# Optimization experiments

Hardware: AMD Instinct MI355X
Metric: run time of the kernel (lower is better)

The kernel has to match this reference:

```python
import jax, jax.numpy as jnp
import numpy as np

DIM = 768
N_HEADS = 12
HEAD_DIM = DIM // N_HEADS
HIDDEN = int(DIM * 4.0)
B, S = 4, 2048
EPS = 1e-6
SCALE = HEAD_DIM ** -0.5


def layer_norm(x, gamma, beta):
    mu = jnp.mean(x, axis=-1, keepdims=True)
    var = jnp.mean((x - mu) ** 2, axis=-1, keepdims=True)
    return (x - mu) * jax.lax.rsqrt(var + EPS) * gamma + beta


def setup_inputs() -> dict:
    key = jax.random.key(0)
    ks = jax.random.split(key, 8)
    x = jax.random.normal(ks[0], (B, S, DIM), dtype=jnp.float32)
    mask = jax.random.randint(ks[1], (B, 1, S, S), 0, 2, dtype=jnp.int32)
    sd = DIM ** -0.5
    return {
        "x": x,
        "mask": mask,
        "w_qkv": jax.random.normal(ks[2], (DIM, 3 * DIM), dtype=jnp.float32) * sd,
        "b_qkv": jnp.zeros((3 * DIM,), jnp.float32),
        "w_proj": jax.random.normal(ks[3], (DIM, DIM), dtype=jnp.float32) * sd,
        "b_proj": jnp.zeros((DIM,), jnp.float32),
        "g1": jnp.ones((DIM,), jnp.float32),
        "beta1": jnp.zeros((DIM,), jnp.float32),
        "g2": jnp.ones((DIM,), jnp.float32),
        "beta2": jnp.zeros((DIM,), jnp.float32),
        "w1": jax.random.normal(ks[4], (DIM, HIDDEN), dtype=jnp.float32) * sd,
        "b1": jnp.zeros((HIDDEN,), jnp.float32),
        "w2": jax.random.normal(ks[5], (HIDDEN, DIM), dtype=jnp.float32) * (HIDDEN ** -0.5),
        "b2": jnp.zeros((DIM,), jnp.float32),
    }


def reference(x, mask, w_qkv, b_qkv, w_proj, b_proj, g1, beta1, g2, beta2, w1, b1, w2, b2):
    # --- attention branch (pre-LN) ---
    h = layer_norm(x, g1, beta1)
    qkv = h @ w_qkv + b_qkv                              # (B,S,3*DIM)
    qkv = qkv.reshape(B, S, 3, N_HEADS, HEAD_DIM)
    q, k, v = (qkv[:, :, 0], qkv[:, :, 1], qkv[:, :, 2])  # (B,S,H,D)
    # scores: (B,H,S,S) -- materialized like the original
    dp = jnp.einsum("bqhd,bkhd->bhqk", q, k) * SCALE
    dp = jnp.where(mask == 0, jnp.float32(-10000.0), dp)
    attn = jax.nn.softmax(dp, axis=-1)
    wa = jnp.einsum("bhqk,bkhd->bqhd", attn, v).reshape(B, S, DIM)
    x = x + (wa @ w_proj + b_proj)
    # --- MLP branch (pre-LN) ---
    h = layer_norm(x, g2, beta2)
    h = jax.nn.gelu(h @ w1 + b1, approximate=False)
    x = x + (h @ w2 + b2)
    return x
```

## Files before the change

### kernel.cpp

```cpp
#include <hip/hip_runtime.h>
#include <hip/hip_bf16.h>
#include <math.h>

typedef __bf16 bf16;
typedef __bf16 bf16x8 __attribute__((ext_vector_type(8)));
typedef short bf16x4s __attribute__((ext_vector_type(4)));
typedef float f32x4 __attribute__((ext_vector_type(4)));

#define DIM 768
#define NH 12
#define HD 64
#define HID 3072
#define BB 4
#define SS 2048
#define QPRESCALE 0.18033688011112042f

#define MFMA(a, b, c) __builtin_amdgcn_mfma_f32_16x16x32_bf16(a, b, c, 0, 0, 0)
#define MFMA16(a, b, c) \
  __builtin_amdgcn_mfma_f32_16x16x16bf16_1k(a, b, c, 0, 0, 0)

__device__ __forceinline__ void gld16(const void* g, void* l) {
  __builtin_amdgcn_global_load_lds(
      (const __attribute__((address_space(1))) void*)g,
      (__attribute__((address_space(3))) void*)l, 16, 0, 0);
}

__device__ __forceinline__ unsigned pk2(float a, float b) {
  union {
    bf16 h[2];
    unsigned u;
  } t;
  t.h[0] = (bf16)a;
  t.h[1] = (bf16)b;
  return t.u;
}

__global__ __launch_bounds__(256) void castT_all_kernel(
    const float* __restrict__ s0, bf16* __restrict__ d0,
    const float* __restrict__ s1, bf16* __restrict__ d1,
    const float* __restrict__ s2, bf16* __restrict__ d2,
    const float* __restrict__ s3, bf16* __restrict__ d3) {
  __shared__ float tile[32][33];
  int id = blockIdx.x;
  const float* in;
  bf16* out;
  int R, C, loc;
  if (id < 1728) { in = s0; out = d0; R = 768; C = 2304; loc = id; }
  else if (id < 2304) { in = s1; out = d1; R = 768; C = 768; loc = id - 1728; }
  else if (id < 4608) { in = s2; out = d2; R = 768; C = 3072; loc = id - 2304; }
  else { in = s3; out = d3; R = 3072; C = 768; loc = id - 4608; }
  const int cb = C >> 5;
  const int c0 = (loc % cb) * 32, r0 = (loc / cb) * 32;
  const int tx = threadIdx.x & 31, ty = threadIdx.x >> 5;
#pragma unroll
  for (int i = 0; i < 32; i += 8)
    tile[ty + i][tx] = in[(size_t)(r0 + ty + i) * C + c0 + tx];
  __syncthreads();
#pragma unroll
  for (int i = 0; i < 32; i += 8)
    out[(size_t)(c0 + ty + i) * R + r0 + tx] = (bf16)tile[tx][ty + i];
}

__global__ __launch_bounds__(256) void maskbits_kernel(
    const int* __restrict__ mask, unsigned* __restrict__ bits) {
  const int i = blockIdx.x * 256 + threadIdx.x;
  unsigned long long m = __ballot(mask[i] != 0);
  const int lane = threadIdx.x & 63;
  if (lane == 0) bits[i >> 5] = (unsigned)m;
  else if (lane == 32) bits[i >> 5] = (unsigned)(m >> 32);
}

__global__ __launch_bounds__(256) void ln_kernel(
    const float* __restrict__ x, const float* __restrict__ g,
    const float* __restrict__ beta, bf16* __restrict__ out) {
  const int row = blockIdx.x, t = threadIdx.x;
  const float* xr = x + (size_t)row * DIM;
  float v0 = xr[t], v1 = xr[t + 256], v2 = xr[t + 512];
  float s = v0 + v1 + v2;
  float s2 = v0 * v0 + v1 * v1 + v2 * v2;
#pragma unroll
  for (int d = 1; d < 64; d <<= 1) {
    s += __shfl_xor(s, d);
    s2 += __shfl_xor(s2, d);
  }
  __shared__ float red[8];
  const int wv = t >> 6, lane = t & 63;
  if (lane == 0) { red[wv] = s; red[wv + 4] = s2; }
  __syncthreads();
  s = red[0] + red[1] + red[2] + red[3];
  s2 = red[4] + red[5] + red[6] + red[7];
  const float mu = s * (1.0f / DIM);
  const float var = s2 * (1.0f / DIM) - mu * mu;
  const float r = rsqrtf(var + 1e-6f);
  bf16* o = out + (size_t)row * DIM;
  o[t] = (bf16)((v0 - mu) * r * g[t] + beta[t]);
  o[t + 256] = (bf16)((v1 - mu) * r * g[t + 256] + beta[t + 256]);
  o[t + 512] = (bf16)((v2 - mu) * r * g[t + 512] + beta[t + 512]);
}

enum { EPI_QKV = 0, EPI_PROJ = 1, EPI_FFN1 = 2, EPI_FFN2 = 3 };

template <int EPI, int K>
__global__ __launch_bounds__(256) void gemm_kernel(
    const bf16* __restrict__ A, const bf16* __restrict__ Bt,
    const float* __restrict__ bias, const float* __restrict__ res,
    void* __restrict__ o0, void* __restrict__ o1, void* __restrict__ o2) {
  constexpr int NIT = K / 64;
  __shared__ bf16 As[2][128 * 64];
  __shared__ bf16 Bs[2][64 * 64];
  const int tid = threadIdx.x;
  const int wv = tid >> 6, lane = tid & 63;
  const int quad = lane >> 4, l15 = lane & 15;
  const int lrow = lane >> 3, lcol = lane & 7;
  const int m0 = blockIdx.y * 128, n0 = blockIdx.x * 64;
  const int wm = wv * 32;

  f32x4 acc[2][4] = {};

  const int swz = (lcol ^ lrow) * 8;
  const bf16* Ag = A + (size_t)(m0 + wv * 32 + lrow) * K + swz;
  const bf16* Bg = Bt + (size_t)(n0 + wv * 16 + lrow) * K + swz;

  auto stage = [&](int buf, int k0) {
#pragma unroll
    for (int i = 0; i < 4; i++)
      gld16(Ag + (size_t)(i * 8) * K + k0, &As[buf][(wv * 32 + i * 8) * 64]);
#pragma unroll
    for (int i = 0; i < 2; i++)
      gld16(Bg + (size_t)(i * 8) * K + k0,
            &Bs[buf][(wv * 16 + i * 8) * 64]);
  };

  stage(0, 0);

  for (int it = 0; it < NIT; ++it) {
    __syncthreads();
    if (it + 1 < NIT) stage((it + 1) & 1, (it + 1) * 64);
    const bf16* Ab = As[it & 1];
    const bf16* Bb = Bs[it & 1];
#pragma unroll
    for (int ks = 0; ks < 2; ks++) {
      bf16x8 af[2], bfr[4];
#pragma unroll
      for (int i = 0; i < 2; i++) {
        const int ra = wm + i * 16 + l15;
        af[i] = *(const bf16x8*)&Ab[ra * 64 + ((ks * 4 + quad) ^ (ra & 7)) * 8];
      }
#pragma unroll
      for (int i = 0; i < 4; i++) {
        const int rb = i * 16 + l15;
        bfr[i] =
            *(const bf16x8*)&Bb[rb * 64 + ((ks * 4 + quad) ^ (rb & 7)) * 8];
      }
#pragma unroll
      for (int mi = 0; mi < 2; mi++)
#pragma unroll
        for (int ni = 0; ni < 4; ni++)
          acc[mi][ni] = MFMA(af[mi], bfr[ni], acc[mi][ni]);
    }
  }

#pragma unroll
  for (int mi = 0; mi < 2; mi++) {
#pragma unroll
    for (int ni = 0; ni < 4; ni++) {
      const int n = n0 + ni * 16 + l15;
      const float bv = bias[n];
      const int mb = m0 + wm + mi * 16 + quad * 4;
      float val[4];
#pragma unroll
      for (int r = 0; r < 4; r++) val[r] = acc[mi][ni][r] + bv;
      if (EPI == EPI_QKV) {
        const int which = n / 768;
        const int nn = n - which * 768;
        const int hh = nn >> 6, d = nn & 63;
        const int bb = mb >> 11, s = mb & 2047;
        if (which == 0) {
#pragma unroll
          for (int r = 0; r < 4; r++)
            ((bf16*)o0)[((size_t)(bb * NH + hh) * SS + s + r) * HD + d] =
                (bf16)(val[r] * QPRESCALE);
        } else if (which == 1) {
#pragma unroll
          for (int r = 0; r < 4; r++)
            ((bf16*)o1)[((size_t)(bb * NH + hh) * SS + s + r) * HD + d] =
                (bf16)val[r];
        } else {
          uint2 pv;
          pv.x = pk2(val[0], val[1]);
          pv.y = pk2(val[2], val[3]);
          *(uint2*)&((bf16*)o2)[((size_t)(bb * NH + hh) * HD + d) * SS + s] = pv;
        }
      } else if (EPI == EPI_PROJ) {
#pragma unroll
        for (int r = 0; r < 4; r++)
          ((float*)o0)[(size_t)(mb + r) * DIM + n] =
              res[(size_t)(mb + r) * DIM + n] + val[r];
      } else if (EPI == EPI_FFN1) {
#pragma unroll
        for (int r = 0; r < 4; r++) {
          const float ge =
              0.5f * val[r] * (1.0f + erff(val[r] * 0.70710678118654752f));
          ((bf16*)o0)[(size_t)(mb + r) * HID + n] = (bf16)ge;
        }
      } else {
#pragma unroll
        for (int r = 0; r < 4; r++)
          ((float*)o0)[(size_t)(mb + r) * DIM + n] =
              res[(size_t)(mb + r) * DIM + n] + val[r];
      }
    }
  }
}

__global__ __launch_bounds__(256) void attn_kernel(
    const bf16* __restrict__ q, const bf16* __restrict__ k,
    const bf16* __restrict__ vT, const unsigned* __restrict__ bits,
    bf16* __restrict__ wa) {
  const int b = blockIdx.z, h = blockIdx.y, q0 = blockIdx.x * 128;
  const int tid = threadIdx.x, wv = tid >> 6, lane = tid & 63;
  const int quad = lane >> 4, l15 = lane & 15;
  const int lrow = lane >> 3, lcol = lane & 7;

  __shared__ bf16 Ks[64 * 64];
  __shared__ bf16 Vs[64 * 64];
  __shared__ unsigned lut[32];

  if (tid < 16) {
    lut[2 * tid] =
        ((tid & 1) ? 0xFFFFu : 0u) | ((tid & 2) ? 0xFFFF0000u : 0u);
    lut[2 * tid + 1] =
        ((tid & 4) ? 0xFFFFu : 0u) | ((tid & 8) ? 0xFFFF0000u : 0u);
  }

  const bf16* qbh = q + (size_t)(b * NH + h) * SS * HD;
  const bf16* kbh = k + (size_t)(b * NH + h) * SS * HD;
  const bf16* vbh = vT + (size_t)(b * NH + h) * HD * SS;

  bf16x8 aq[2][2];
#pragma unroll
  for (int mi = 0; mi < 2; mi++)
#pragma unroll
    for (int ks = 0; ks < 2; ks++) {
      const int s = q0 + wv * 32 + mi * 16 + l15;
      aq[mi][ks] = *(const bf16x8*)&qbh[(size_t)s * HD + ks * 32 + quad * 8];
    }

  const unsigned long long* mrow[2];
#pragma unroll
  for (int mi = 0; mi < 2; mi++)
    mrow[mi] = (const unsigned long long*)bits +
               (size_t)(b * SS + q0 + wv * 32 + mi * 16 + l15) * 32;

  f32x4 O[2][4] = {};
  f32x4 lm[2] = {};
  const short oneb = 0x3F80;
  const bf16x4s onesA = {oneb, oneb, oneb, oneb};
  const int swz = (lcol ^ lrow) * 8;

  for (int t = 0; t < SS / 64; ++t) {
    const int s0 = t * 64;
#pragma unroll
    for (int i = 0; i < 2; i++) {
      const int r = wv * 16 + i * 8 + lrow;
      gld16(&kbh[(size_t)(s0 + r) * HD + swz], &Ks[(wv * 16 + i * 8) * 64]);
      gld16(&vbh[(size_t)r * SS + s0 + swz], &Vs[(wv * 16 + i * 8) * 64]);
    }
    const unsigned long long sh0 = mrow[0][t] >> (quad * 4);
    const unsigned long long sh1 = mrow[1][t] >> (quad * 4);
    const unsigned lo0 = (unsigned)sh0, hi0 = (unsigned)(sh0 >> 32);
    const unsigned lo1 = (unsigned)sh1, hi1 = (unsigned)(sh1 >> 32);
    __syncthreads();

#pragma unroll
    for (int ni = 0; ni < 4; ni++) {
      const int rr = ni * 16 + l15;
      const bf16x8 kf0 = *(const bf16x8*)&Ks[rr * 64 + (quad ^ (rr & 7)) * 8];
      const bf16x8 kf1 =
          *(const bf16x8*)&Ks[rr * 64 + ((4 + quad) ^ (rr & 7)) * 8];
      f32x4 a0 = {}, a1 = {};
      a0 = MFMA(kf0, aq[0][0], a0);
      a0 = MFMA(kf1, aq[0][1], a0);
      a1 = MFMA(kf0, aq[1][0], a1);
      a1 = MFMA(kf1, aq[1][1], a1);
      const unsigned nib0 = (ni == 0)   ? (lo0 & 0xF)
                            : (ni == 1) ? ((lo0 >> 16) & 0xF)
                            : (ni == 2) ? (hi0 & 0xF)
                                        : ((hi0 >> 16) & 0xF);
      const unsigned nib1 = (ni == 0)   ? (lo1 & 0xF)
                            : (ni == 1) ? ((lo1 >> 16) & 0xF)
                            : (ni == 2) ? (hi1 & 0xF)
                                        : ((hi1 >> 16) & 0xF);
      const uint2 mw0 = *(const uint2*)&lut[2 * nib0];
      const uint2 mw1 = *(const uint2*)&lut[2 * nib1];
      union {
        unsigned u[2];
        bf16x4s v;
      } p0, p1;
      p0.u[0] = pk2(__builtin_amdgcn_exp2f(a0[0]),
                    __builtin_amdgcn_exp2f(a0[1])) & mw0.x;
      p0.u[1] = pk2(__builtin_amdgcn_exp2f(a0[2]),
                    __builtin_amdgcn_exp2f(a0[3])) & mw0.y;
      p1.u[0] = pk2(__builtin_amdgcn_exp2f(a1[0]),
                    __builtin_amdgcn_exp2f(a1[1])) & mw1.x;
      p1.u[1] = pk2(__builtin_amdgcn_exp2f(a1[2]),
                    __builtin_amdgcn_exp2f(a1[3])) & mw1.y;
      lm[0] = MFMA16(onesA, p0.v, lm[0]);
      lm[1] = MFMA16(onesA, p1.v, lm[1]);
#pragma unroll
      for (int nd = 0; nd < 4; nd++) {
        const int row = nd * 16 + l15;
        const int pc = (ni * 2 + (quad >> 1)) ^ (row & 7);
        const bf16x4s vf =
            *(const bf16x4s*)&Vs[row * 64 + pc * 8 + (quad & 1) * 4];
        O[0][nd] = MFMA16(vf, p0.v, O[0][nd]);
        O[1][nd] = MFMA16(vf, p1.v, O[1][nd]);
      }
    }
    __syncthreads();
  }

#pragma unroll
  for (int mi = 0; mi < 2; mi++) {
    const float rln = __builtin_amdgcn_rcpf(lm[mi][0]);
    const int sq = q0 + wv * 32 + mi * 16 + l15;
    bf16* dst = wa + (size_t)(b * SS + sq) * DIM + h * HD + quad * 4;
#pragma unroll
    for (int nd = 0; nd < 4; nd++) {
      uint2 pv;
      pv.x = pk2(O[mi][nd][0] * rln, O[mi][nd][1] * rln);
      pv.y = pk2(O[mi][nd][2] * rln, O[mi][nd][3] * rln);
      *(uint2*)&dst[nd * 16] = pv;
    }
  }
}

extern "C" void kernel_launch(void* const* d_in, const int* in_sizes, int n_in,
                              void* d_out, int out_size, void* d_ws,
                              size_t ws_size, hipStream_t stream) {
  const float* x = (const float*)d_in[0];
  const int* mask = (const int*)d_in[1];
  const float* w_qkv = (const float*)d_in[2];
  const float* b_qkv = (const float*)d_in[3];
  const float* w_proj = (const float*)d_in[4];
  const float* b_proj = (const float*)d_in[5];
  const float* g1 = (const float*)d_in[6];
  const float* beta1 = (const float*)d_in[7];
  const float* g2 = (const float*)d_in[8];
  const float* beta2 = (const float*)d_in[9];
  const float* w1 = (const float*)d_in[10];
  const float* b1 = (const float*)d_in[11];
  const float* w2 = (const float*)d_in[12];
  const float* b2 = (const float*)d_in[13];
  float* out = (float*)d_out;

  char* p = (char*)d_ws;
  auto alloc = [&](size_t bytes) {
    char* r = p;
    p += (bytes + 1023) & ~(size_t)1023;
    return r;
  };
  bf16* wqkvT = (bf16*)alloc((size_t)2304 * 768 * 2);
  bf16* wprojT = (bf16*)alloc((size_t)768 * 768 * 2);
  bf16* w1T = (bf16*)alloc((size_t)3072 * 768 * 2);
  bf16* w2T = (bf16*)alloc((size_t)768 * 3072 * 2);
  unsigned* bits = (unsigned*)alloc((size_t)BB * SS * 64 * 4);
  bf16* h = (bf16*)alloc((size_t)8192 * 768 * 2);
  bf16* qb = (bf16*)alloc((size_t)8192 * 768 * 2);
  bf16* kb = (bf16*)alloc((size_t)8192 * 768 * 2);
  bf16* vtb = (bf16*)alloc((size_t)8192 * 768 * 2);
  bf16* wab = (bf16*)alloc((size_t)8192 * 768 * 2);
  float* x2 = (float*)alloc((size_t)8192 * 768 * 4);
  bf16* ffn1 = (bf16*)alloc((size_t)8192 * 3072 * 2);

  castT_all_kernel<<<6912, 256, 0, stream>>>(w_qkv, wqkvT, w_proj, wprojT, w1,
                                             w1T, w2, w2T);
  maskbits_kernel<<<(BB * SS * SS) / 256, 256, 0, stream>>>(mask, bits);
  ln_kernel<<<8192, 256, 0, stream>>>(x, g1, beta1, h);
  gemm_kernel<EPI_QKV, 768>
      <<<dim3(2304 / 64, 8192 / 128), 256, 0, stream>>>(h, wqkvT, b_qkv,
                                                        nullptr, qb, kb, vtb);
  attn_kernel<<<dim3(SS / 128, NH, BB), 256, 0, stream>>>(qb, kb, vtb, bits,
                                                          wab);
  gemm_kernel<EPI_PROJ, 768>
      <<<dim3(768 / 64, 8192 / 128), 256, 0, stream>>>(wab, wprojT, b_proj, x,
                                                       x2, nullptr, nullptr);
  ln_kernel<<<8192, 256, 0, stream>>>(x2, g2, beta2, h);
  gemm_kernel<EPI_FFN1, 768>
      <<<dim3(3072 / 64, 8192 / 128), 256, 0, stream>>>(h, w1T, b1, nullptr,
                                                        ffn1, nullptr,
                                                        nullptr);
  gemm_kernel<EPI_FFN2, 3072>
      <<<dim3(768 / 64, 8192 / 128), 256, 0, stream>>>(ffn1, w2T, b2, x2, out,
                                                       nullptr, nullptr);
}
```

Baseline: 494.1 us.

## Split attention over key halves with double-buffered KV and reduce kernel; shrink GEMM K-tile

Attention now splits the key dimension in two, doubling the grid. Each half writes unnormalised fp32 partial outputs and row sums, and a new reduce kernel combines and normalises them into bf16. The K/V tiles are double-buffered so the next tile loads while the current one computes, with one barrier per iteration. The GEMM K-tile drops from 64 to 32 with a new swizzle, halving LDS use to raise occupancy but doubling the number of barriers. The risk is the extra fp32 partial-output traffic (about 50 MB) and an added launch. The split-K combine assumes no running max (fixed-scale exp), which holds for the existing design.

After: 544.9 us. 10.3% more time.

```diff
diff --git a/kernel.cpp b/kernel.cpp
--- a/kernel.cpp
+++ b/kernel.cpp
@@ -105,59 +105,53 @@
     const bf16* __restrict__ A, const bf16* __restrict__ Bt,
     const float* __restrict__ bias, const float* __restrict__ res,
     void* __restrict__ o0, void* __restrict__ o1, void* __restrict__ o2) {
-  constexpr int NIT = K / 64;
-  __shared__ bf16 As[2][128 * 64];
-  __shared__ bf16 Bs[2][64 * 64];
+  constexpr int NIT = K / 32;
+  __shared__ bf16 As[2][128 * 32];
+  __shared__ bf16 Bs[2][64 * 32];
   const int tid = threadIdx.x;
   const int wv = tid >> 6, lane = tid & 63;
   const int quad = lane >> 4, l15 = lane & 15;
-  const int lrow = lane >> 3, lcol = lane & 7;
+  const int l2 = lane >> 2, c4 = lane & 3, ssw = (lane >> 3) & 3;
   const int m0 = blockIdx.y * 128, n0 = blockIdx.x * 64;
   const int wm = wv * 32;
 
   f32x4 acc[2][4] = {};
 
-  const int swz = (lcol ^ lrow) * 8;
-  const bf16* Ag = A + (size_t)(m0 + wv * 32 + lrow) * K + swz;
-  const bf16* Bg = Bt + (size_t)(n0 + wv * 16 + lrow) * K + swz;
+  const int gch = (c4 ^ ssw) * 8;
+  const bf16* Ag = A + (size_t)(m0 + wv * 32 + l2) * K + gch;
+  const bf16* Bg = Bt + (size_t)(n0 + wv * 16 + l2) * K + gch;
 
   auto stage = [&](int buf, int k0) {
-#pragma unroll
-    for (int i = 0; i < 4; i++)
-      gld16(Ag + (size_t)(i * 8) * K + k0, &As[buf][(wv * 32 + i * 8) * 64]);
-#pragma unroll
-    for (int i = 0; i < 2; i++)
-      gld16(Bg + (size_t)(i * 8) * K + k0,
-            &Bs[buf][(wv * 16 + i * 8) * 64]);
+    gld16(Ag + k0, &As[buf][(wv * 32) * 32]);
+    gld16(Ag + (size_t)16 * K + k0, &As[buf][(wv * 32 + 16) * 32]);
+    gld16(Bg + k0, &Bs[buf][(wv * 16) * 32]);
   };
 
   stage(0, 0);
+  const int fsw = (l15 >> 1) & 3;
+  const int pch = ((quad ^ fsw) & 3) * 8;
 
   for (int it = 0; it < NIT; ++it) {
     __syncthreads();
-    if (it + 1 < NIT) stage((it + 1) & 1, (it + 1) * 64);
+    if (it + 1 < NIT) stage((it + 1) & 1, (it + 1) * 32);
     const bf16* Ab = As[it & 1];
     const bf16* Bb = Bs[it & 1];
-#pragma unroll
-    for (int ks = 0; ks < 2; ks++) {
-      bf16x8 af[2], bfr[4];
-#pragma unroll
-      for (int i = 0; i < 2; i++) {
-        const int ra = wm + i * 16 + l15;
-        af[i] = *(const bf16x8*)&Ab[ra * 64 + ((ks * 4 + quad) ^ (ra & 7)) * 8];
-      }
-#pragma unroll
-      for (int i = 0; i < 4; i++) {
-        const int rb = i * 16 + l15;
-        bfr[i] =
-            *(const bf16x8*)&Bb[rb * 64 + ((ks * 4 + quad) ^ (rb & 7)) * 8];
-      }
-#pragma unroll
-      for (int mi = 0; mi < 2; mi++)
-#pragma unroll
-        for (int ni = 0; ni < 4; ni++)
-          acc[mi][ni] = MFMA(af[mi], bfr[ni], acc[mi][ni]);
-    }
+    bf16x8 af[2], bfr[4];
+#pragma unroll
+    for (int i = 0; i < 2; i++) {
+      const int ra = wm + i * 16 + l15;
+      af[i] = *(const bf16x8*)&Ab[ra * 32 + pch];
+    }
+#pragma unroll
+    for (int i = 0; i < 4; i++) {
+      const int rb = i * 16 + l15;
+      bfr[i] = *(const bf16x8*)&Bb[rb * 32 + pch];
+    }
+#pragma unroll
+    for (int mi = 0; mi < 2; mi++)
+#pragma unroll
+      for (int ni = 0; ni < 4; ni++)
+        acc[mi][ni] = MFMA(af[mi], bfr[ni], acc[mi][ni]);
   }
 
 #pragma unroll
@@ -216,14 +210,16 @@
 __global__ __launch_bounds__(256) void attn_kernel(
     const bf16* __restrict__ q, const bf16* __restrict__ k,
     const bf16* __restrict__ vT, const unsigned* __restrict__ bits,
-    bf16* __restrict__ wa) {
-  const int b = blockIdx.z, h = blockIdx.y, q0 = blockIdx.x * 128;
+    float* __restrict__ Opart, float* __restrict__ Lpart) {
+  const int b = blockIdx.z, h = blockIdx.y;
+  const int ksl = blockIdx.x & 1, q0 = (blockIdx.x >> 1) * 128;
+  const int kbase = ksl * (SS / 2);
   const int tid = threadIdx.x, wv = tid >> 6, lane = tid & 63;
   const int quad = lane >> 4, l15 = lane & 15;
   const int lrow = lane >> 3, lcol = lane & 7;
 
-  __shared__ bf16 Ks[64 * 64];
-  __shared__ bf16 Vs[64 * 64];
+  __shared__ bf16 Ks[2][64 * 64];
+  __shared__ bf16 Vs[2][64 * 64];
   __shared__ unsigned lut[32];
 
   if (tid < 16) {
@@ -250,7 +246,8 @@
 #pragma unroll
   for (int mi = 0; mi < 2; mi++)
     mrow[mi] = (const unsigned long long*)bits +
-               (size_t)(b * SS + q0 + wv * 32 + mi * 16 + l15) * 32;
+               (size_t)(b * SS + q0 + wv * 32 + mi * 16 + l15) * 32 +
+               (kbase >> 6);
 
   f32x4 O[2][4] = {};
   f32x4 lm[2] = {};
@@ -258,26 +255,35 @@
   const bf16x4s onesA = {oneb, oneb, oneb, oneb};
   const int swz = (lcol ^ lrow) * 8;
 
-  for (int t = 0; t < SS / 64; ++t) {
-    const int s0 = t * 64;
+  auto stageKV = [&](int buf, int s0) {
 #pragma unroll
     for (int i = 0; i < 2; i++) {
       const int r = wv * 16 + i * 8 + lrow;
-      gld16(&kbh[(size_t)(s0 + r) * HD + swz], &Ks[(wv * 16 + i * 8) * 64]);
-      gld16(&vbh[(size_t)r * SS + s0 + swz], &Vs[(wv * 16 + i * 8) * 64]);
-    }
+      gld16(&kbh[(size_t)(s0 + r) * HD + swz],
+            &Ks[buf][(wv * 16 + i * 8) * 64]);
+      gld16(&vbh[(size_t)r * SS + s0 + swz],
+            &Vs[buf][(wv * 16 + i * 8) * 64]);
+    }
+  };
+
+  stageKV(0, kbase);
+
+  for (int t = 0; t < 16; ++t) {
+    __syncthreads();
+    if (t + 1 < 16) stageKV((t + 1) & 1, kbase + (t + 1) * 64);
+    const bf16* Kc = Ks[t & 1];
+    const bf16* Vc = Vs[t & 1];
     const unsigned long long sh0 = mrow[0][t] >> (quad * 4);
     const unsigned long long sh1 = mrow[1][t] >> (quad * 4);
     const unsigned lo0 = (unsigned)sh0, hi0 = (unsigned)(sh0 >> 32);
     const unsigned lo1 = (unsigned)sh1, hi1 = (unsigned)(sh1 >> 32);
-    __syncthreads();
 
 #pragma unroll
     for (int ni = 0; ni < 4; ni++) {
       const int rr = ni * 16 + l15;
-      const bf16x8 kf0 = *(const bf16x8*)&Ks[rr * 64 + (quad ^ (rr & 7)) * 8];
+      const bf16x8 kf0 = *(const bf16x8*)&Kc[rr * 64 + (quad ^ (rr & 7)) * 8];
       const bf16x8 kf1 =
-          *(const bf16x8*)&Ks[rr * 64 + ((4 + quad) ^ (rr & 7)) * 8];
+          *(const bf16x8*)&Kc[rr * 64 + ((4 + quad) ^ (rr & 7)) * 8];
       f32x4 a0 = {}, a1 = {};
       a0 = MFMA(kf0, aq[0][0], a0);
       a0 = MFMA(kf1, aq[0][1], a0);
@@ -312,26 +318,43 @@
         const int row = nd * 16 + l15;
         const int pc = (ni * 2 + (quad >> 1)) ^ (row & 7);
         const bf16x4s vf =
-            *(const bf16x4s*)&Vs[row * 64 + pc * 8 + (quad & 1) * 4];
+            *(const bf16x4s*)&Vc[row * 64 + pc * 8 + (quad & 1) * 4];
         O[0][nd] = MFMA16(vf, p0.v, O[0][nd]);
         O[1][nd] = MFMA16(vf, p1.v, O[1][nd]);
       }
     }
-    __syncthreads();
   }
 
 #pragma unroll
   for (int mi = 0; mi < 2; mi++) {
-    const float rln = __builtin_amdgcn_rcpf(lm[mi][0]);
     const int sq = q0 + wv * 32 + mi * 16 + l15;
-    bf16* dst = wa + (size_t)(b * SS + sq) * DIM + h * HD + quad * 4;
+    float* od = Opart + ((size_t)ksl * BB * SS + (size_t)b * SS + sq) * DIM +
+                h * HD + quad * 4;
 #pragma unroll
     for (int nd = 0; nd < 4; nd++) {
-      uint2 pv;
-      pv.x = pk2(O[mi][nd][0] * rln, O[mi][nd][1] * rln);
-      pv.y = pk2(O[mi][nd][2] * rln, O[mi][nd][3] * rln);
-      *(uint2*)&dst[nd * 16] = pv;
-    }
+      f32x4 o = O[mi][nd];
+      *(f32x4*)&od[nd * 16] = o;
+    }
+    if (quad == 0)
+      Lpart[(((size_t)ksl * BB + b) * NH + h) * SS + sq] = lm[mi][0];
+  }
+}
+
+__global__ __launch_bounds__(256) void attn_reduce_kernel(
+    const float* __restrict__ Op, const float* __restrict__ Lp,
+    bf16* __restrict__ wa) {
+  const int row = blockIdx.x;
+  const int b = row >> 11, s = row & 2047;
+  const int t = threadIdx.x;
+#pragma unroll
+  for (int j = 0; j < 3; j++) {
+    const int d = t + j * 256;
+    const int h = d >> 6;
+    const float l = Lp[((size_t)b * NH + h) * SS + s] +
+                    Lp[(((size_t)BB + b) * NH + h) * SS + s];
+    const float o = Op[(size_t)row * DIM + d] +
+                    Op[((size_t)BB * SS + row) * DIM + d];
+    wa[(size_t)row * DIM + d] = (bf16)(o * __builtin_amdgcn_rcpf(l));
   }
 }
 
@@ -372,6 +395,8 @@
   bf16* wab = (bf16*)alloc((size_t)8192 * 768 * 2);
   float* x2 = (float*)alloc((size_t)8192 * 768 * 4);
   bf16* ffn1 = (bf16*)alloc((size_t)8192 * 3072 * 2);
+  float* Opart = (float*)alloc((size_t)2 * 8192 * 768 * 4);
+  float* Lpart = (float*)alloc((size_t)2 * BB * NH * SS * 4);
 
   castT_all_kernel<<<6912, 256, 0, stream>>>(w_qkv, wqkvT, w_proj, wprojT, w1,
                                              w1T, w2, w2T);
@@ -380,8 +405,9 @@
   gemm_kernel<EPI_QKV, 768>
       <<<dim3(2304 / 64, 8192 / 128), 256, 0, stream>>>(h, wqkvT, b_qkv,
                                                         nullptr, qb, kb, vtb);
-  attn_kernel<<<dim3(SS / 128, NH, BB), 256, 0, stream>>>(qb, kb, vtb, bits,
-                                                          wab);
+  attn_kernel<<<dim3((SS / 128) * 2, NH, BB), 256, 0, stream>>>(
+      qb, kb, vtb, bits, Opart, Lpart);
+  attn_reduce_kernel<<<BB * SS, 256, 0, stream>>>(Opart, Lpart, wab);
   gemm_kernel<EPI_PROJ, 768>
       <<<dim3(768 / 64, 8192 / 128), 256, 0, stream>>>(wab, wprojT, b_proj, x,
                                                        x2, nullptr, nullptr);
```

## Double-buffer K/V tiles in attention and use smaller M tiles for narrow GEMMs

Applied to the files above, without the earlier changes.

The attention kernel now double-buffers its K and V shared-memory tiles, prefetching the next tile while the current one is computed, and needs only one barrier per iteration. The GEMM kernel gains a TM template parameter, and the PROJ and FFN2 GEMMs (N=768) use 64-row tiles, doubling their block count to fill more compute units. The cost is twice the LDS in attention, which can lower occupancy, and less A/B reuse per block in the smaller-tile GEMMs.

New measurement: 514.5 us. 4.1% more time.

```diff
diff --git a/kernel.cpp b/kernel.cpp
--- a/kernel.cpp
+++ b/kernel.cpp
@@ -100,35 +100,36 @@
 
 enum { EPI_QKV = 0, EPI_PROJ = 1, EPI_FFN1 = 2, EPI_FFN2 = 3 };
 
-template <int EPI, int K>
+template <int EPI, int K, int TM>
 __global__ __launch_bounds__(256) void gemm_kernel(
     const bf16* __restrict__ A, const bf16* __restrict__ Bt,
     const float* __restrict__ bias, const float* __restrict__ res,
     void* __restrict__ o0, void* __restrict__ o1, void* __restrict__ o2) {
   constexpr int NIT = K / 64;
-  __shared__ bf16 As[2][128 * 64];
+  constexpr int MI = TM / 64;
+  constexpr int RPW = TM / 4;
+  __shared__ bf16 As[2][TM * 64];
   __shared__ bf16 Bs[2][64 * 64];
   const int tid = threadIdx.x;
   const int wv = tid >> 6, lane = tid & 63;
   const int quad = lane >> 4, l15 = lane & 15;
   const int lrow = lane >> 3, lcol = lane & 7;
-  const int m0 = blockIdx.y * 128, n0 = blockIdx.x * 64;
-  const int wm = wv * 32;
-
-  f32x4 acc[2][4] = {};
+  const int m0 = blockIdx.y * TM, n0 = blockIdx.x * 64;
+  const int wm = wv * RPW;
+
+  f32x4 acc[MI][4] = {};
 
   const int swz = (lcol ^ lrow) * 8;
-  const bf16* Ag = A + (size_t)(m0 + wv * 32 + lrow) * K + swz;
+  const bf16* Ag = A + (size_t)(m0 + wv * RPW + lrow) * K + swz;
   const bf16* Bg = Bt + (size_t)(n0 + wv * 16 + lrow) * K + swz;
 
   auto stage = [&](int buf, int k0) {
 #pragma unroll
-    for (int i = 0; i < 4; i++)
-      gld16(Ag + (size_t)(i * 8) * K + k0, &As[buf][(wv * 32 + i * 8) * 64]);
+    for (int i = 0; i < RPW / 8; i++)
+      gld16(Ag + (size_t)(i * 8) * K + k0, &As[buf][(wv * RPW + i * 8) * 64]);
 #pragma unroll
     for (int i = 0; i < 2; i++)
-      gld16(Bg + (size_t)(i * 8) * K + k0,
-            &Bs[buf][(wv * 16 + i * 8) * 64]);
+      gld16(Bg + (size_t)(i * 8) * K + k0, &Bs[buf][(wv * 16 + i * 8) * 64]);
   };
 
   stage(0, 0);
@@ -140,9 +141,9 @@
     const bf16* Bb = Bs[it & 1];
 #pragma unroll
     for (int ks = 0; ks < 2; ks++) {
-      bf16x8 af[2], bfr[4];
-#pragma unroll
-      for (int i = 0; i < 2; i++) {
+      bf16x8 af[MI], bfr[4];
+#pragma unroll
+      for (int i = 0; i < MI; i++) {
         const int ra = wm + i * 16 + l15;
         af[i] = *(const bf16x8*)&Ab[ra * 64 + ((ks * 4 + quad) ^ (ra & 7)) * 8];
       }
@@ -153,7 +154,7 @@
             *(const bf16x8*)&Bb[rb * 64 + ((ks * 4 + quad) ^ (rb & 7)) * 8];
       }
 #pragma unroll
-      for (int mi = 0; mi < 2; mi++)
+      for (int mi = 0; mi < MI; mi++)
 #pragma unroll
         for (int ni = 0; ni < 4; ni++)
           acc[mi][ni] = MFMA(af[mi], bfr[ni], acc[mi][ni]);
@@ -161,7 +162,7 @@
   }
 
 #pragma unroll
-  for (int mi = 0; mi < 2; mi++) {
+  for (int mi = 0; mi < MI; mi++) {
 #pragma unroll
     for (int ni = 0; ni < 4; ni++) {
       const int n = n0 + ni * 16 + l15;
@@ -222,8 +223,8 @@
   const int quad = lane >> 4, l15 = lane & 15;
   const int lrow = lane >> 3, lcol = lane & 7;
 
-  __shared__ bf16 Ks[64 * 64];
-  __shared__ bf16 Vs[64 * 64];
+  __shared__ bf16 Ks[2][64 * 64];
+  __shared__ bf16 Vs[2][64 * 64];
   __shared__ unsigned lut[32];
 
   if (tid < 16) {
@@ -258,26 +259,35 @@
   const bf16x4s onesA = {oneb, oneb, oneb, oneb};
   const int swz = (lcol ^ lrow) * 8;
 
-  for (int t = 0; t < SS / 64; ++t) {
-    const int s0 = t * 64;
+  auto stageKV = [&](int buf, int s0) {
 #pragma unroll
     for (int i = 0; i < 2; i++) {
       const int r = wv * 16 + i * 8 + lrow;
-      gld16(&kbh[(size_t)(s0 + r) * HD + swz], &Ks[(wv * 16 + i * 8) * 64]);
-      gld16(&vbh[(size_t)r * SS + s0 + swz], &Vs[(wv * 16 + i * 8) * 64]);
-    }
+      gld16(&kbh[(size_t)(s0 + r) * HD + swz],
+            &Ks[buf][(wv * 16 + i * 8) * 64]);
+      gld16(&vbh[(size_t)r * SS + s0 + swz],
+            &Vs[buf][(wv * 16 + i * 8) * 64]);
+    }
+  };
+
+  stageKV(0, 0);
+
+  for (int t = 0; t < SS / 64; ++t) {
+    __syncthreads();
+    if (t + 1 < SS / 64) stageKV((t + 1) & 1, (t + 1) * 64);
+    const bf16* Kc = Ks[t & 1];
+    const bf16* Vc = Vs[t & 1];
     const unsigned long long sh0 = mrow[0][t] >> (quad * 4);
     const unsigned long long sh1 = mrow[1][t] >> (quad * 4);
     const unsigned lo0 = (unsigned)sh0, hi0 = (unsigned)(sh0 >> 32);
     const unsigned lo1 = (unsigned)sh1, hi1 = (unsigned)(sh1 >> 32);
-    __syncthreads();
 
 #pragma unroll
     for (int ni = 0; ni < 4; ni++) {
       const int rr = ni * 16 + l15;
-      const bf16x8 kf0 = *(const bf16x8*)&Ks[rr * 64 + (quad ^ (rr & 7)) * 8];
+      const bf16x8 kf0 = *(const bf16x8*)&Kc[rr * 64 + (quad ^ (rr & 7)) * 8];
       const bf16x8 kf1 =
-          *(const bf16x8*)&Ks[rr * 64 + ((4 + quad) ^ (rr & 7)) * 8];
+          *(const bf16x8*)&Kc[rr * 64 + ((4 + quad) ^ (rr & 7)) * 8];
       f32x4 a0 = {}, a1 = {};
       a0 = MFMA(kf0, aq[0][0], a0);
       a0 = MFMA(kf1, aq[0][1], a0);
@@ -312,12 +322,11 @@
         const int row = nd * 16 + l15;
         const int pc = (ni * 2 + (quad >> 1)) ^ (row & 7);
         const bf16x4s vf =
-            *(const bf16x4s*)&Vs[row * 64 + pc * 8 + (quad & 1) * 4];
+            *(const bf16x4s*)&Vc[row * 64 + pc * 8 + (quad & 1) * 4];
         O[0][nd] = MFMA16(vf, p0.v, O[0][nd]);
         O[1][nd] = MFMA16(vf, p1.v, O[1][nd]);
       }
     }
-    __syncthreads();
   }
 
 #pragma unroll
@@ -377,20 +386,20 @@
                                              w1T, w2, w2T);
   maskbits_kernel<<<(BB * SS * SS) / 256, 256, 0, stream>>>(mask, bits);
   ln_kernel<<<8192, 256, 0, stream>>>(x, g1, beta1, h);
-  gemm_kernel<EPI_QKV, 768>
+  gemm_kernel<EPI_QKV, 768, 128>
       <<<dim3(2304 / 64, 8192 / 128), 256, 0, stream>>>(h, wqkvT, b_qkv,
                                                         nullptr, qb, kb, vtb);
   attn_kernel<<<dim3(SS / 128, NH, BB), 256, 0, stream>>>(qb, kb, vtb, bits,
                                                           wab);
-  gemm_kernel<EPI_PROJ, 768>
-      <<<dim3(768 / 64, 8192 / 128), 256, 0, stream>>>(wab, wprojT, b_proj, x,
-                                                       x2, nullptr, nullptr);
+  gemm_kernel<EPI_PROJ, 768, 64>
+      <<<dim3(768 / 64, 8192 / 64), 256, 0, stream>>>(wab, wprojT, b_proj, x,
+                                                      x2, nullptr, nullptr);
   ln_kernel<<<8192, 256, 0, stream>>>(x2, g2, beta2, h);
-  gemm_kernel<EPI_FFN1, 768>
+  gemm_kernel<EPI_FFN1, 768, 128>
       <<<dim3(3072 / 64, 8192 / 128), 256, 0, stream>>>(h, w1T, b1, nullptr,
                                                         ffn1, nullptr,
                                                         nullptr);
-  gemm_kernel<EPI_FFN2, 3072>
-      <<<dim3(768 / 64, 8192 / 128), 256, 0, stream>>>(ffn1, w2T, b2, x2, out,
-                                                       nullptr, nullptr);
-}
+  gemm_kernel<EPI_FFN2, 3072, 64>
+      <<<dim3(768 / 64, 8192 / 64), 256, 0, stream>>>(ffn1, w2T, b2, x2, out,
+                                                      nullptr, nullptr);
+}
```
